# Performance work log

Measured on AMD Instinct MI355X. Metric: run time of the kernel, lower is better.

Reference implementation:

```python
import jax, jax.numpy as jnp
import numpy as np
from jax import lax

B, L, HID, H, KS, C = 2, 4096, 1024, 4, 4, 64
DH = HID // H
EPS = 1e-5


def setup_inputs():
    key = jax.random.key(0)
    ks = jax.random.split(key, 10)
    s = 0.02
    return {
        "x": jax.random.normal(ks[0], (B, L, HID), jnp.float32),
        "Wq": jax.random.normal(ks[1], (HID, HID), jnp.float32) * s,
        "Wk": jax.random.normal(ks[2], (HID, HID), jnp.float32) * s,
        "Wv": jax.random.normal(ks[3], (HID, HID), jnp.float32) * s,
        "conv_q": jax.random.normal(ks[4], (HID, 1, KS), jnp.float32) * 0.3,
        "conv_k": jax.random.normal(ks[5], (HID, 1, KS), jnp.float32) * 0.3,
        "conv_v": jax.random.normal(ks[6], (HID, 1, KS), jnp.float32) * 0.3,
        "Wbeta": jax.random.normal(ks[7], (H, HID), jnp.float32) * s,
        "rms_w": jnp.ones((HID,), jnp.float32),
        "Wo": jax.random.normal(ks[8], (HID, HID), jnp.float32) * s,
    }


def _silu(x):
    return x * jax.nn.sigmoid(x)


def _conv_act(x, w):
    # depthwise causal conv1d: torch pads both sides by KS-1 then truncates to L,
    # which equals left-pad KS-1 + valid conv. Then SiLU (as in _calculate_conv).
    y = lax.conv_general_dilated(x.transpose(0, 2, 1), w, (1,), [(KS - 1, 0)],
                                 feature_group_count=HID,
                                 dimension_numbers=('NCH', 'OIH', 'NCH'))
    return _silu(y).transpose(0, 2, 1)


def _l2norm(x):
    # matches F.normalize(p=2, dim=-1) with eps=1e-12
    return x / jnp.maximum(jnp.linalg.norm(x, axis=-1, keepdims=True), 1e-12)


def _chunk_delta_rule(Q, K, V, beta):
    b, l, h, d = Q.shape
    n = (l + C - 1) // C
    pad = n * C - l
    if pad:
        padw = ((0, 0), (0, pad), (0, 0), (0, 0))
        Q, K, V, beta = (jnp.pad(a, padw) for a in (Q, K, V, beta))
    Q, K, V = (a.reshape(b, n, C, h, d) for a in (Q, K, V))
    beta = beta.reshape(b, n, C, h, 1)
    Kb, Vb = K * beta, V * beta
    # T is SUMMED over heads in the source (single shared T per chunk).
    T = -jnp.tril(jnp.einsum('bnihd,bnjhd->bnij', Kb, K), -1) + jnp.eye(C, dtype=Q.dtype)
    # forward-substitution UT transform: T[i,:i] += T[i,:] @ T[:, :i], sequentially in i
    def body(i, T):
        row = T[:, :, i, :]                                  # (b,n,C)
        prod = jnp.einsum('bnj,bnjc->bnc', row, T)
        new = jnp.where(jnp.arange(C) < i, row + prod, row)
        return T.at[:, :, i, :].set(new)
    T = lax.fori_loop(1, C, body, T)
    W = jnp.einsum('bnij,bnjhd->bnihd', T, Kb)
    U = jnp.einsum('bnij,bnjhd->bnihd', T, Vb)

    def step(S, inp):
        q_i, k_i, w_i, u0 = inp                              # each (b,C,h,d)
        # torch.einsum('bchd,bhdd->bchd', ., S) extracts diag(S) (repeated 'd')
        dS = jnp.einsum('bhdd->bhd', S)
        u_i = u0 - w_i * dS[:, None]
        o_inter = q_i * dS[:, None]
        # source: A_i = einsum('bchd,bchd->bc', q, k).tril()  (tril over batch/chunk dims!)
        A = jnp.tril(jnp.einsum('bchd,bchd->bc', q_i, k_i))
        o_intra = jnp.einsum('bc,bchd->bchd', A, u_i)
        S = S + jnp.einsum('bchd,bche->bhde', k_i, u_i)
        return S, o_inter + o_intra

    S0 = jnp.zeros((b, h, d, d), Q.dtype)
    mv = lambda a: jnp.moveaxis(a, 1, 0)                     # chunks to scan axis
    S, O = lax.scan(step, S0, (mv(Q), mv(K), mv(W), mv(U)))
    O = jnp.moveaxis(O, 0, 1).reshape(b, n * C, h, d)[:, :l]
    return O, S


def _forward(x, Wq, Wk, Wv, conv_q, conv_k, conv_v, Wbeta, rms_w, Wo):
    q = _conv_act(x @ Wq.T, conv_q).reshape(B, L, H, DH)
    k = _conv_act(x @ Wk.T, conv_k).reshape(B, L, H, DH)
    v = _conv_act(x @ Wv.T, conv_v).reshape(B, L, H, DH)
    q, k, v = _silu(q), _silu(k), _silu(v)                   # second SiLU, as in source
    q, k = _l2norm(q), _l2norm(k)
    beta = jax.nn.sigmoid(x @ Wbeta.T)[..., None]            # (B,L,H,1)
    o, S = _chunk_delta_rule(q, k, v, beta)
    o = o.reshape(B, L, HID)
    o = o * lax.rsqrt(jnp.mean(o * o, axis=-1, keepdims=True) + EPS) * rms_w
    return o @ Wo.T, S


def reference(x, Wq, Wk, Wv, conv_q, conv_k, conv_v, Wbeta, rms_w, Wo):
    return _forward(x, Wq, Wk, Wv, conv_q, conv_k, conv_v, Wbeta, rms_w, Wo)
```

## Files before the change

### kernel.cpp

```cpp
#include <hip/hip_runtime.h>
#include <hip/hip_bf16.h>

#define L_SEQ 4096
#define HID 1024
#define NH 4
#define DH 256
#define CK 64
#define BL_TOT 8192

typedef short v8s __attribute__((ext_vector_type(8)));
typedef unsigned short v8u __attribute__((ext_vector_type(8)));
typedef unsigned short v4us __attribute__((ext_vector_type(4)));
typedef float v4f __attribute__((ext_vector_type(4)));

typedef __attribute__((address_space(1))) const void* as1cv;
typedef __attribute__((address_space(3))) void* as3v;

__device__ __forceinline__ unsigned short f2bu(float f) {
    __hip_bfloat16 h = __float2bfloat16(f);
    return *(unsigned short*)&h;
}
__device__ __forceinline__ float bu2f(unsigned short u) {
    __hip_bfloat16 h = *(__hip_bfloat16*)&u;
    return __bfloat162float(h);
}
__device__ __forceinline__ void storec(float* p, float v) { *p = v; }
__device__ __forceinline__ void storec(unsigned short* p, float v) { *p = f2bu(v); }

__global__ __launch_bounds__(256) void wcvt_kernel(const float* __restrict__ s0, const float* __restrict__ s1,
                                                   const float* __restrict__ s2, const float* __restrict__ s3,
                                                   unsigned short* __restrict__ d0, unsigned short* __restrict__ d1,
                                                   unsigned short* __restrict__ d2, unsigned short* __restrict__ d3) {
    const float* s = blockIdx.y == 0 ? s0 : blockIdx.y == 1 ? s1 : blockIdx.y == 2 ? s2 : s3;
    unsigned short* d = blockIdx.y == 0 ? d0 : blockIdx.y == 1 ? d1 : blockIdx.y == 2 ? d2 : d3;
    int i = blockIdx.x * 256 + threadIdx.x;
    int stride = gridDim.x * 256;
    for (; i < HID * HID; i += stride) d[i] = f2bu(s[i]);
}

template <typename OT>
__global__ __launch_bounds__(256) void gemm_mfma(const unsigned short* __restrict__ Ah,
                                                 const unsigned short* __restrict__ Bh,
                                                 OT* __restrict__ C, int M, int N, int K) {
    __shared__ unsigned short AsH[128 * 32];
    __shared__ unsigned short BsH[128 * 32];
    const int tid = threadIdx.x;
    const int wave = tid >> 6, lane = tid & 63;
    const int quad = lane >> 4, l16 = lane & 15;
    const int m0 = blockIdx.x * 128, n0 = blockIdx.y * 128;
    const int wm = (wave >> 1) * 64, wn = (wave & 1) * 64;

    const int srow = wave * 16 + (lane >> 2);
    const int scol = (((lane & 3) ^ ((srow >> 1) & 3)) * 8);
    const unsigned short* Ag = Ah + (size_t)(m0 + srow) * K + scol;
    const unsigned short* Bg = Bh + (size_t)(n0 + srow) * K + scol;
    char* lA = (char*)AsH;
    char* lB = (char*)BsH;
    const int lbase = wave * 1024;
    const int qsw = (quad ^ ((l16 >> 1) & 3)) * 8;

    v4f acc[4][4];
#pragma unroll
    for (int a = 0; a < 4; ++a)
#pragma unroll
        for (int b = 0; b < 4; ++b) { v4f z = {0.f, 0.f, 0.f, 0.f}; acc[a][b] = z; }

    for (int k0 = 0; k0 < K; k0 += 32) {
        __syncthreads();
        __builtin_amdgcn_global_load_lds((as1cv)(Ag + k0), (as3v)(lA + lbase), 16, 0, 0);
        __builtin_amdgcn_global_load_lds((as1cv)(Ag + (size_t)64 * K + k0), (as3v)(lA + 4096 + lbase), 16, 0, 0);
        __builtin_amdgcn_global_load_lds((as1cv)(Bg + k0), (as3v)(lB + lbase), 16, 0, 0);
        __builtin_amdgcn_global_load_lds((as1cv)(Bg + (size_t)64 * K + k0), (as3v)(lB + 4096 + lbase), 16, 0, 0);
        __syncthreads();
        v8s afh[4], bfh[4];
#pragma unroll
        for (int mt = 0; mt < 4; ++mt) afh[mt] = *(const v8s*)&AsH[(wm + mt * 16 + l16) * 32 + qsw];
#pragma unroll
        for (int nt = 0; nt < 4; ++nt) bfh[nt] = *(const v8s*)&BsH[(wn + nt * 16 + l16) * 32 + qsw];
#pragma unroll
        for (int mt = 0; mt < 4; ++mt)
#pragma unroll
            for (int nt = 0; nt < 4; ++nt)
                acc[mt][nt] = __builtin_amdgcn_mfma_f32_16x16x32_bf16(afh[mt], bfh[nt], acc[mt][nt], 0, 0, 0);
    }
#pragma unroll
    for (int mt = 0; mt < 4; ++mt)
#pragma unroll
        for (int nt = 0; nt < 4; ++nt) {
            int row = m0 + wm + mt * 16 + quad * 4;
            int col = n0 + wn + nt * 16 + l16;
#pragma unroll
            for (int r = 0; r < 4; ++r)
                storec(&C[(size_t)(row + r) * N + col], acc[mt][nt][r]);
        }
}

__global__ __launch_bounds__(256) void beta_kernel(const float* __restrict__ x,
                                                   const float* __restrict__ Wb,
                                                   float* __restrict__ betaB,
                                                   unsigned short* __restrict__ xh) {
    const int t = blockIdx.x;
    const int tid = threadIdx.x;
    const int wave = tid >> 6, lane = tid & 63;
    const float* xr = x + (size_t)t * HID;
    v4f xv = *(const v4f*)(xr + tid * 4);
    v4us xp;
#pragma unroll
    for (int i = 0; i < 4; ++i) xp[i] = f2bu(xv[i]);
    *(v4us*)&xh[(size_t)t * HID + tid * 4] = xp;
    float s[4];
#pragma unroll
    for (int h = 0; h < 4; ++h) {
        v4f wv = *(const v4f*)(Wb + (size_t)h * HID + tid * 4);
        s[h] = xv[0] * wv[0] + xv[1] * wv[1] + xv[2] * wv[2] + xv[3] * wv[3];
    }
#pragma unroll
    for (int off = 32; off; off >>= 1)
#pragma unroll
        for (int h = 0; h < 4; ++h) s[h] += __shfl_down(s[h], off);
    __shared__ float red[4][4];
    if (lane == 0)
#pragma unroll
        for (int h = 0; h < 4; ++h) red[wave][h] = s[h];
    __syncthreads();
    if (tid < 4) {
        float tot = red[0][tid] + red[1][tid] + red[2][tid] + red[3][tid];
        betaB[(size_t)t * 4 + tid] = 1.f / (1.f + expf(-tot));
    }
}

__global__ __launch_bounds__(256) void conv_kernel(const unsigned short* __restrict__ G, int gstride, int pathArg,
                                                   const float* __restrict__ wq, const float* __restrict__ wk,
                                                   const float* __restrict__ wv,
                                                   unsigned short* __restrict__ Vout,
                                                   unsigned short* __restrict__ KhiO, unsigned short* __restrict__ KloO,
                                                   unsigned short* __restrict__ Qout) {
    const int p = pathArg < 0 ? (int)blockIdx.y : pathArg;
    const int yoff = pathArg < 0 ? p * 1024 : 0;
    const float* __restrict__ w = p == 0 ? wv : p == 1 ? wk : wq;
    const int bl = blockIdx.x;
    const int l = bl & (L_SEQ - 1);
    const int tid = threadIdx.x;
    const int lane = tid & 63;
    const int c4 = (tid >> 6) * 256 + lane * 4;
    v4f wrow[4];
#pragma unroll
    for (int cc = 0; cc < 4; ++cc) wrow[cc] = *(const v4f*)&w[(c4 + cc) * 4];
    v4f acc = {0.f, 0.f, 0.f, 0.f};
#pragma unroll
    for (int j = 0; j < 4; ++j) {
        int ls = l - 3 + j;
        if (ls >= 0) {
            v4us g = *(const v4us*)&G[(size_t)(bl - 3 + j) * gstride + yoff + c4];
#pragma unroll
            for (int cc = 0; cc < 4; ++cc) acc[cc] += bu2f(g[cc]) * wrow[cc][j];
        }
    }
    float vals[4];
#pragma unroll
    for (int cc = 0; cc < 4; ++cc) {
        float a = acc[cc];
        float s1 = a / (1.f + expf(-a));
        vals[cc] = s1 / (1.f + expf(-s1));
    }
    if (p >= 1) {
        float sq = vals[0] * vals[0] + vals[1] * vals[1] + vals[2] * vals[2] + vals[3] * vals[3];
#pragma unroll
        for (int off = 32; off; off >>= 1) sq += __shfl_xor(sq, off);
        float nrm = 1.f / fmaxf(sqrtf(sq), 1e-12f);
#pragma unroll
        for (int cc = 0; cc < 4; ++cc) vals[cc] *= nrm;
    }
    const size_t ob = (size_t)bl * HID + c4;
    if (p == 1) {
        v4us hv, lv;
#pragma unroll
        for (int cc = 0; cc < 4; ++cc) {
            unsigned short h = f2bu(vals[cc]);
            hv[cc] = h;
            lv[cc] = f2bu(vals[cc] - bu2f(h));
        }
        *(v4us*)&KhiO[ob] = hv;
        *(v4us*)&KloO[ob] = lv;
    } else {
        unsigned short* O = p == 0 ? Vout : Qout;
        v4us hv;
#pragma unroll
        for (int cc = 0; cc < 4; ++cc) hv[cc] = f2bu(vals[cc]);
        *(v4us*)&O[ob] = hv;
    }
}

__global__ __launch_bounds__(256) void gram_kernel(const unsigned short* __restrict__ Khi,
                                                   const unsigned short* __restrict__ Klo,
                                                   float* __restrict__ Gg) {
    const int chunk = blockIdx.x;
    const int h = blockIdx.y;
    const int tid = threadIdx.x;
    const int wave = tid >> 6, lane = tid & 63;
    const int quad = lane >> 4, l16 = lane & 15;
    __shared__ unsigned short Hs[64 * 264];
    __shared__ unsigned short Ls[64 * 264];
    const int l0 = chunk * 64;
    const int cb = h * 256;
#pragma unroll
    for (int p = 0; p < 8; ++p) {
        int row = p * 8 + (tid >> 5);
        int col = (tid & 31) * 8;
        v8u hv = *(const v8u*)(Khi + (size_t)(l0 + row) * HID + cb + col);
        v8u lv = *(const v8u*)(Klo + (size_t)(l0 + row) * HID + cb + col);
        *(v8u*)&Hs[row * 264 + col] = hv;
        *(v8u*)&Ls[row * 264 + col] = lv;
    }
    __syncthreads();
    const int wm = wave * 16;
    v4f acc[4];
#pragma unroll
    for (int nt = 0; nt < 4; ++nt) { v4f z = {0.f, 0.f, 0.f, 0.f}; acc[nt] = z; }
#pragma unroll
    for (int ks = 0; ks < 8; ++ks) {
        v8s ah = *(const v8s*)&Hs[(wm + l16) * 264 + ks * 32 + quad * 8];
        v8s al = *(const v8s*)&Ls[(wm + l16) * 264 + ks * 32 + quad * 8];
#pragma unroll
        for (int nt = 0; nt < 4; ++nt) {
            v8s bh = *(const v8s*)&Hs[(nt * 16 + l16) * 264 + ks * 32 + quad * 8];
            v8s bl = *(const v8s*)&Ls[(nt * 16 + l16) * 264 + ks * 32 + quad * 8];
            acc[nt] = __builtin_amdgcn_mfma_f32_16x16x32_bf16(ah, bh, acc[nt], 0, 0, 0);
            acc[nt] = __builtin_amdgcn_mfma_f32_16x16x32_bf16(ah, bl, acc[nt], 0, 0, 0);
            acc[nt] = __builtin_amdgcn_mfma_f32_16x16x32_bf16(al, bh, acc[nt], 0, 0, 0);
        }
    }
    float* og = Gg + ((size_t)chunk * 4 + h) * 4096;
#pragma unroll
    for (int nt = 0; nt < 4; ++nt)
#pragma unroll
        for (int r = 0; r < 4; ++r)
            og[(wm + quad * 4 + r) * 64 + nt * 16 + l16] = acc[nt][r];
}

__global__ __launch_bounds__(256) void trec_kernel(const float* __restrict__ Gg,
                                                   const float* __restrict__ betaB,
                                                   float* __restrict__ Tg) {
    const int chunk = blockIdx.x;
    const int tid = threadIdx.x;
    const int wave = tid >> 6, lane = tid & 63;
    const int quad = lane >> 4, l16 = lane & 15;
    const int wm = wave * 16;
    __shared__ unsigned short BhR[64 * 72], BlR[64 * 72];
    __shared__ unsigned short BhT[64 * 72], BlT[64 * 72];
    __shared__ unsigned short PhR[64 * 72], PlR[64 * 72];
    __shared__ float Pf[64 * 73];
    __shared__ float betS[256];
    betS[tid] = betaB[(size_t)chunk * 256 + tid];
    __syncthreads();
    const float* gg = Gg + (size_t)chunk * 4 * 4096;
#pragma unroll
    for (int s = 0; s < 16; ++s) {
        int idx = tid + 256 * s;
        int i = idx >> 6, j = idx & 63;
        float a = 0.f;
        if (i > j) {
            a = -(betS[i * 4 + 0] * gg[idx] + betS[i * 4 + 1] * gg[4096 + idx] +
                  betS[i * 4 + 2] * gg[2 * 4096 + idx] + betS[i * 4 + 3] * gg[3 * 4096 + idx]);
        }
        unsigned short ah = f2bu(a);
        unsigned short al = f2bu(a - bu2f(ah));
        BhR[i * 72 + j] = ah;
        BlR[i * 72 + j] = al;
        BhT[j * 72 + i] = ah;
        BlT[j * 72 + i] = al;
        float p = (i == j) ? 1.f : 0.f;
        Pf[i * 73 + j] = p;
        PhR[i * 72 + j] = f2bu(p);
        PlR[i * 72 + j] = 0;
    }
    __syncthreads();

    for (int st = 0; st < 6; ++st) {
        v8s aBh[2], aBl[2], aPh[2], aPl[2];
        v8s bTh[2][4], bTl[2][4];
#pragma unroll
        for (int kk = 0; kk < 2; ++kk) {
            aBh[kk] = *(const v8s*)&BhR[(wm + l16) * 72 + kk * 32 + quad * 8];
            aBl[kk] = *(const v8s*)&BlR[(wm + l16) * 72 + kk * 32 + quad * 8];
            aPh[kk] = *(const v8s*)&PhR[(wm + l16) * 72 + kk * 32 + quad * 8];
            aPl[kk] = *(const v8s*)&PlR[(wm + l16) * 72 + kk * 32 + quad * 8];
#pragma unroll
            for (int nt = 0; nt < 4; ++nt) {
                bTh[kk][nt] = *(const v8s*)&BhT[(nt * 16 + l16) * 72 + kk * 32 + quad * 8];
                bTl[kk][nt] = *(const v8s*)&BlT[(nt * 16 + l16) * 72 + kk * 32 + quad * 8];
            }
        }
        v4f accP[4], accB[4];
#pragma unroll
        for (int nt = 0; nt < 4; ++nt) {
#pragma unroll
            for (int r = 0; r < 4; ++r)
                accP[nt][r] = Pf[(wm + quad * 4 + r) * 73 + nt * 16 + l16];
            v4f z = {0.f, 0.f, 0.f, 0.f};
            accB[nt] = z;
        }
        __syncthreads();
#pragma unroll
        for (int kk = 0; kk < 2; ++kk)
#pragma unroll
            for (int nt = 0; nt < 4; ++nt) {
                accP[nt] = __builtin_amdgcn_mfma_f32_16x16x32_bf16(aPh[kk], bTh[kk][nt], accP[nt], 0, 0, 0);
                accP[nt] = __builtin_amdgcn_mfma_f32_16x16x32_bf16(aPh[kk], bTl[kk][nt], accP[nt], 0, 0, 0);
                accP[nt] = __builtin_amdgcn_mfma_f32_16x16x32_bf16(aPl[kk], bTh[kk][nt], accP[nt], 0, 0, 0);
            }
        if (st < 5) {
#pragma unroll
            for (int kk = 0; kk < 2; ++kk)
#pragma unroll
                for (int nt = 0; nt < 4; ++nt) {
                    accB[nt] = __builtin_amdgcn_mfma_f32_16x16x32_bf16(aBh[kk], bTh[kk][nt], accB[nt], 0, 0, 0);
                    accB[nt] = __builtin_amdgcn_mfma_f32_16x16x32_bf16(aBh[kk], bTl[kk][nt], accB[nt], 0, 0, 0);
                    accB[nt] = __builtin_amdgcn_mfma_f32_16x16x32_bf16(aBl[kk], bTh[kk][nt], accB[nt], 0, 0, 0);
                }
        }
#pragma unroll
        for (int nt = 0; nt < 4; ++nt)
#pragma unroll
            for (int r = 0; r < 4; ++r) {
                int row = wm + quad * 4 + r;
                int col = nt * 16 + l16;
                float pv = accP[nt][r];
                Pf[row * 73 + col] = pv;
                unsigned short ph = f2bu(pv);
                PhR[row * 72 + col] = ph;
                PlR[row * 72 + col] = f2bu(pv - bu2f(ph));
                if (st < 5) {
                    float bv = accB[nt][r];
                    unsigned short bh2 = f2bu(bv);
                    unsigned short bl2 = f2bu(bv - bu2f(bh2));
                    BhR[row * 72 + col] = bh2;
                    BlR[row * 72 + col] = bl2;
                    BhT[col * 72 + row] = bh2;
                    BlT[col * 72 + row] = bl2;
                }
            }
        __syncthreads();
    }
#pragma unroll
    for (int s = 0; s < 16; ++s) {
        int idx = tid + 256 * s;
        int i = idx >> 6, j = idx & 63;
        float t = (i == j) ? 1.f : 3.f * Pf[i * 73 + j];
        Tg[(size_t)chunk * 4096 + idx] = t;
    }
}

__global__ __launch_bounds__(256) void wu_mfma_kernel(const float* __restrict__ Tg,
                                                      const unsigned short* __restrict__ Khi,
                                                      const unsigned short* __restrict__ Vhi,
                                                      const float* __restrict__ betaB,
                                                      unsigned short* __restrict__ Wb,
                                                      unsigned short* __restrict__ Ub,
                                                      float* __restrict__ kw, float* __restrict__ ku) {
    const int chunk = blockIdx.x;
    const int h = blockIdx.y;
    const int half = blockIdx.z;
    const int tid = threadIdx.x;
    const int wave = tid >> 6, lane = tid & 63;
    const int quad = lane >> 4, l16 = lane & 15;
    const size_t l0 = (size_t)chunk * 64;
    const int f0 = h * 256 + half * 128;
    __shared__ unsigned short Th[64 * 72], Tl[64 * 72];
    __shared__ unsigned short KT[128 * 72], VT[128 * 72];
    __shared__ float betS[64];
    if (tid < 64) betS[tid] = betaB[(l0 + tid) * 4 + h];
    __syncthreads();
#pragma unroll
    for (int s = 0; s < 16; ++s) {
        int idx = tid + 256 * s;
        int c = idx >> 6, j = idx & 63;
        float v = Tg[(size_t)chunk * 4096 + idx] * betS[j];
        unsigned short hv = f2bu(v);
        Th[c * 72 + j] = hv;
        Tl[c * 72 + j] = f2bu(v - bu2f(hv));
    }
#pragma unroll
    for (int pass = 0; pass < 4; ++pass) {
        int j = pass * 16 + (tid >> 4);
        int fc = (tid & 15) * 8;
        v8u kv = *(const v8u*)(Khi + (l0 + j) * HID + f0 + fc);
        v8u vv = *(const v8u*)(Vhi + (l0 + j) * HID + f0 + fc);
#pragma unroll
        for (int i = 0; i < 8; ++i) {
            KT[(fc + i) * 72 + j] = kv[i];
            VT[(fc + i) * 72 + j] = vv[i];
        }
    }
    __syncthreads();

    const int nf = wave * 32;
    const int bb = chunk >> 6, nn = chunk & 63;
    const size_t obase = (((size_t)bb * 4 + h) * 64 + nn) * 256 + half * 128;

#pragma unroll
    for (int phase = 0; phase < 2; ++phase) {
        const unsigned short* BT = phase ? VT : KT;
        v4f acc[4][2];
#pragma unroll
        for (int mt = 0; mt < 4; ++mt)
#pragma unroll
            for (int nt = 0; nt < 2; ++nt) { v4f z = {0.f, 0.f, 0.f, 0.f}; acc[mt][nt] = z; }
#pragma unroll
        for (int k0 = 0; k0 < 64; k0 += 32) {
            v8s ah[4], al[4], bf[2];
#pragma unroll
            for (int mt = 0; mt < 4; ++mt) {
                ah[mt] = *(const v8s*)&Th[(mt * 16 + l16) * 72 + k0 + quad * 8];
                al[mt] = *(const v8s*)&Tl[(mt * 16 + l16) * 72 + k0 + quad * 8];
            }
#pragma unroll
            for (int nt = 0; nt < 2; ++nt)
                bf[nt] = *(const v8s*)&BT[(nf + nt * 16 + l16) * 72 + k0 + quad * 8];
#pragma unroll
            for (int mt = 0; mt < 4; ++mt)
#pragma unroll
                for (int nt = 0; nt < 2; ++nt) {
                    acc[mt][nt] = __builtin_amdgcn_mfma_f32_16x16x32_bf16(ah[mt], bf[nt], acc[mt][nt], 0, 0, 0);
                    acc[mt][nt] = __builtin_amdgcn_mfma_f32_16x16x32_bf16(al[mt], bf[nt], acc[mt][nt], 0, 0, 0);
                }
        }
        unsigned short* Out = phase ? Ub : Wb;
        float* kk = phase ? ku : kw;
#pragma unroll
        for (int nt = 0; nt < 2; ++nt) {
            const int fl = nf + nt * 16 + l16;
            float dot = 0.f;
#pragma unroll
            for (int mt = 0; mt < 4; ++mt)
#pragma unroll
                for (int r = 0; r < 4; ++r) {
                    const int c = mt * 16 + quad * 4 + r;
                    float wv = acc[mt][nt][r];
                    Out[(l0 + c) * HID + f0 + fl] = f2bu(wv);
                    dot += bu2f(KT[fl * 72 + c]) * wv;
                }
            dot += __shfl_xor(dot, 16);
            dot += __shfl_xor(dot, 32);
            if (quad == 0) kk[obase + fl] = dot;
        }
    }
}

__global__ __launch_bounds__(256) void scan_kernel(const float* __restrict__ kw,
                                                   const float* __restrict__ ku,
                                                   float* __restrict__ dsA) {
    const int bh = blockIdx.x;
    const int e = threadIdx.x;
    float ds = 0.f;
    for (int n = 0; n < 64; ++n) {
        size_t idx = ((size_t)bh * 64 + n) * 256 + e;
        dsA[idx] = ds;
        ds = ds * (1.f - kw[idx]) + ku[idx];
    }
}

__device__ __forceinline__ float block_sum(float v, float* red) {
#pragma unroll
    for (int off = 32; off; off >>= 1) v += __shfl_down(v, off);
    const int wave = threadIdx.x >> 6;
    if ((threadIdx.x & 63) == 0) red[wave] = v;
    __syncthreads();
    float t = red[0] + red[1] + red[2] + red[3];
    __syncthreads();
    return t;
}

__global__ __launch_bounds__(256) void o_kernel(const unsigned short* __restrict__ Qb,
                                                const unsigned short* __restrict__ Khi,
                                                const unsigned short* __restrict__ Wb,
                                                const unsigned short* __restrict__ Ub,
                                                const float* __restrict__ dsA,
                                                const float* __restrict__ rmsw,
                                                unsigned short* __restrict__ ob,
                                                unsigned short* __restrict__ ub) {
    const int bl = blockIdx.x;
    const int b = bl >> 12, l = bl & (L_SEQ - 1);
    const int n = l >> 6, cpos = l & 63;
    const int tid = threadIdx.x;
    const int hh = tid >> 6, le = (tid & 63) * 4;
    const int c4 = hh * 256 + le;
    __shared__ float red[4];
    const size_t rowb = (size_t)bl * HID;
    v4f dsv = *(const v4f*)&dsA[(((size_t)b * 4 + hh) * 64 + n) * 256 + le];
    v4us qu = *(const v4us*)&Qb[rowb + c4];
    float qv[4];
#pragma unroll
    for (int i = 0; i < 4; ++i) qv[i] = bu2f(qu[i]);
    const bool doA = (cpos <= b);
    float Aval = 0.f;
    if (doA) {
        v4us kq = *(const v4us*)&Khi[rowb + c4];
        float s = 0.f;
#pragma unroll
        for (int i = 0; i < 4; ++i) s += qv[i] * bu2f(kq[i]);
        Aval = block_sum(s, red);
    }
    v4us uu = *(const v4us*)&Ub[rowb + c4];
    v4us wu4 = *(const v4us*)&Wb[rowb + c4];
    float ss = 0.f, ov[4];
    v4us up;
#pragma unroll
    for (int i = 0; i < 4; ++i) {
        float u = bu2f(uu[i]) - bu2f(wu4[i]) * dsv[i];
        up[i] = f2bu(u);
        float o = qv[i] * dsv[i];
        if (doA) o += Aval * u;
        ov[i] = o;
        ss += o * o;
    }
    *(v4us*)&ub[rowb + c4] = up;
    float tot = block_sum(ss, red);
    float scale = rsqrtf(tot * (1.f / 1024.f) + 1e-5f);
    v4f rw = *(const v4f*)&rmsw[c4];
    v4us op;
#pragma unroll
    for (int i = 0; i < 4; ++i) op[i] = f2bu(ov[i] * scale * rw[i]);
    *(v4us*)&ob[rowb + c4] = op;
}

#define SNS 8
__global__ __launch_bounds__(256) void s_mfma_kernel(const unsigned short* __restrict__ Khi,
                                                     const unsigned short* __restrict__ Ub,
                                                     float* __restrict__ Spart) {
    const int bh = blockIdx.x;
    const int b = bh >> 2, h = bh & 3;
    const int dt = blockIdx.y;
    const int et = blockIdx.z & 1;
    const int ns = blockIdx.z >> 1;
    const int tid = threadIdx.x;
    const int wave = tid >> 6, lane = tid & 63;
    const int quad = lane >> 4, l16 = lane & 15;
    const int wm = (wave >> 1) * 64, wn = (wave & 1) * 64;
    __shared__ unsigned short Kt[128 * 40];
    __shared__ unsigned short Ut[128 * 40];
    const int cc = tid >> 3;
    const int dcol = (tid & 7) * 16;
    const size_t rowbase = (size_t)b * 4096 + (size_t)ns * 512;
    const int ck = h * 256 + dt * 128;
    const int ce = h * 256 + et * 128;
    v4f acc[4][4];
#pragma unroll
    for (int a = 0; a < 4; ++a)
#pragma unroll
        for (int c2 = 0; c2 < 4; ++c2) { v4f z = {0.f, 0.f, 0.f, 0.f}; acc[a][c2] = z; }

    for (int kt = 0; kt < 16; ++kt) {
        size_t row = rowbase + kt * 32 + cc;
        v8u k0 = *(const v8u*)(Khi + row * HID + ck + dcol);
        v8u k1 = *(const v8u*)(Khi + row * HID + ck + dcol + 8);
        v8u u0 = *(const v8u*)(Ub + row * HID + ce + dcol);
        v8u u1 = *(const v8u*)(Ub + row * HID + ce + dcol + 8);
        __syncthreads();
#pragma unroll
        for (int j = 0; j < 8; ++j) {
            Kt[(dcol + j) * 40 + cc] = k0[j];
            Kt[(dcol + 8 + j) * 40 + cc] = k1[j];
            Ut[(dcol + j) * 40 + cc] = u0[j];
            Ut[(dcol + 8 + j) * 40 + cc] = u1[j];
        }
        __syncthreads();
        v8s af[4], bf[4];
#pragma unroll
        for (int mt = 0; mt < 4; ++mt) af[mt] = *(const v8s*)&Kt[(wm + mt * 16 + l16) * 40 + quad * 8];
#pragma unroll
        for (int nt = 0; nt < 4; ++nt) bf[nt] = *(const v8s*)&Ut[(wn + nt * 16 + l16) * 40 + quad * 8];
#pragma unroll
        for (int mt = 0; mt < 4; ++mt)
#pragma unroll
            for (int nt = 0; nt < 4; ++nt)
                acc[mt][nt] = __builtin_amdgcn_mfma_f32_16x16x32_bf16(af[mt], bf[nt], acc[mt][nt], 0, 0, 0);
    }
    float* out = Spart + (size_t)ns * (8 * 256 * 256);
#pragma unroll
    for (int mt = 0; mt < 4; ++mt)
#pragma unroll
        for (int nt = 0; nt < 4; ++nt) {
            int row = dt * 128 + wm + mt * 16 + quad * 4;
            int col = et * 128 + wn + nt * 16 + l16;
#pragma unroll
            for (int r = 0; r < 4; ++r)
                out[((size_t)bh * 256 + row + r) * 256 + col] = acc[mt][nt][r];
        }
}

__global__ __launch_bounds__(256) void sreduce_kernel(const float* __restrict__ Spart,
                                                      float* __restrict__ out) {
    int i = blockIdx.x * 256 + threadIdx.x;
    float s = 0.f;
#pragma unroll
    for (int ns = 0; ns < SNS; ++ns) s += Spart[(size_t)ns * (8 * 256 * 256) + i];
    out[i] = s;
}

extern "C" void kernel_launch(void* const* d_in, const int* in_sizes, int n_in,
                              void* d_out, int out_size, void* d_ws, size_t ws_size,
                              hipStream_t stream) {
    const float* x     = (const float*)d_in[0];
    const float* Wq    = (const float*)d_in[1];
    const float* Wk    = (const float*)d_in[2];
    const float* Wv    = (const float*)d_in[3];
    const float* convq = (const float*)d_in[4];
    const float* convk = (const float*)d_in[5];
    const float* convv = (const float*)d_in[6];
    const float* Wbeta = (const float*)d_in[7];
    const float* rmsw  = (const float*)d_in[8];
    const float* Wo    = (const float*)d_in[9];

    char* ws = (char*)d_ws;
    size_t off = 0;
    auto alloc = [&](size_t bytes) {
        char* p = ws + off;
        off += (bytes + 255) & ~(size_t)255;
        return (void*)p;
    };
    const size_t MM = (size_t)HID * HID;
    unsigned short* xhi   = (unsigned short*)alloc((size_t)BL_TOT * HID * 2);
    unsigned short* Khi   = (unsigned short*)alloc((size_t)BL_TOT * HID * 2);
    unsigned short* wbQKV = (unsigned short*)alloc(3 * MM * 2);
    unsigned short* wbO   = (unsigned short*)alloc(MM * 2);
    unsigned short* Vhi   = (unsigned short*)alloc((size_t)BL_TOT * HID * 2);
    unsigned short* Wb16  = (unsigned short*)alloc((size_t)BL_TOT * HID * 2);
    unsigned short* Ub16  = (unsigned short*)alloc((size_t)BL_TOT * HID * 2);
    float* Tg    = (float*)alloc((size_t)128 * 4096 * 4);
    float* betaB = (float*)alloc((size_t)BL_TOT * 4 * 4);
    float* kwB   = (float*)alloc((size_t)8 * 64 * 256 * 4);
    float* kuB   = (float*)alloc((size_t)8 * 64 * 256 * 4);
    float* dsA   = (float*)alloc((size_t)8 * 64 * 256 * 4);
    const size_t gt_big = (size_t)BL_TOT * 3 * HID * 2;
    const size_t gt_small = (size_t)BL_TOT * HID * 2;
    const size_t spart_bytes = (size_t)SNS * 8 * 256 * 256 * 4;
    const bool big = (off + (gt_big > spart_bytes ? gt_big : spart_bytes)) <= ws_size;
    unsigned short* Gt = (unsigned short*)alloc(big ? (gt_big > spart_bytes ? gt_big : spart_bytes)
                                                    : (gt_small > spart_bytes ? gt_small : spart_bytes));

    unsigned short* Qm = xhi;
    unsigned short* ob = Qm;
    float* Spart = (float*)Gt;

    float* out0 = (float*)d_out;
    float* out1 = out0 + (size_t)BL_TOT * HID;
    unsigned short* Klo = (unsigned short*)out0;
    unsigned short* ubf = (unsigned short*)out0 + 8388608;
    float* Gg = out0 + (size_t)4400000;

    dim3 blk(256);
    dim3 ggrid(BL_TOT / 128, HID / 128);

    wcvt_kernel<<<dim3(256, 4), blk, 0, stream>>>(Wv, Wk, Wq, Wo, wbQKV, wbQKV + MM, wbQKV + 2 * MM, wbO);
    beta_kernel<<<BL_TOT, blk, 0, stream>>>(x, Wbeta, betaB, xhi);

    if (big) {
        gemm_mfma<unsigned short><<<dim3(BL_TOT / 128, 3 * HID / 128), blk, 0, stream>>>(
            xhi, wbQKV, Gt, BL_TOT, 3 * HID, HID);
        conv_kernel<<<dim3(BL_TOT, 3), blk, 0, stream>>>(Gt, 3 * HID, -1, convq, convk, convv,
                                                         Vhi, Khi, Klo, Qm);
        gram_kernel<<<dim3(128, 4), blk, 0, stream>>>(Khi, Klo, Gg);
        trec_kernel<<<128, blk, 0, stream>>>(Gg, betaB, Tg);
    } else {
        gemm_mfma<unsigned short><<<ggrid, blk, 0, stream>>>(xhi, wbQKV, Gt, BL_TOT, HID, HID);
        conv_kernel<<<dim3(BL_TOT, 1), blk, 0, stream>>>(Gt, HID, 0, convq, convk, convv, Vhi, Khi, Klo, Qm);
        gemm_mfma<unsigned short><<<ggrid, blk, 0, stream>>>(xhi, wbQKV + MM, Gt, BL_TOT, HID, HID);
        conv_kernel<<<dim3(BL_TOT, 1), blk, 0, stream>>>(Gt, HID, 1, convq, convk, convv, Vhi, Khi, Klo, Qm);
        gram_kernel<<<dim3(128, 4), blk, 0, stream>>>(Khi, Klo, Gg);
        trec_kernel<<<128, blk, 0, stream>>>(Gg, betaB, Tg);
        gemm_mfma<unsigned short><<<ggrid, blk, 0, stream>>>(xhi, wbQKV + 2 * MM, Gt, BL_TOT, HID, HID);
        conv_kernel<<<dim3(BL_TOT, 1), blk, 0, stream>>>(Gt, HID, 2, convq, convk, convv, Vhi, Khi, Klo, Qm);
    }

    wu_mfma_kernel<<<dim3(128, 4, 2), blk, 0, stream>>>(Tg, Khi, Vhi, betaB, Wb16, Ub16, kwB, kuB);
    scan_kernel<<<8, blk, 0, stream>>>(kwB, kuB, dsA);
    o_kernel<<<BL_TOT, blk, 0, stream>>>(Qm, Khi, Wb16, Ub16, dsA, rmsw, ob, ubf);
    s_mfma_kernel<<<dim3(8, 2, 2 * SNS), blk, 0, stream>>>(Khi, ubf, Spart);
    sreduce_kernel<<<2048, blk, 0, stream>>>(Spart, out1);

    gemm_mfma<float><<<ggrid, blk, 0, stream>>>(ob, wbO, out0, BL_TOT, HID, HID);
}
```

Before: 369.9 us.

## Double GEMM K-tile to 64 and use one wave per row in beta/o kernels

The bf16 MFMA GEMM now stages 64-wide K tiles with a new 8-way XOR swizzle, halving the number of barrier pairs per K loop at the cost of twice the LDS per block. The beta and output-norm kernels are restructured so each wave handles a full row, replacing block-level shared-memory reductions and __syncthreads with wave shuffles and launching a quarter as many blocks. These changes target barrier and launch overhead in the GEMMs and the row-wise elementwise kernels, but they raise per-thread register use.

```diff
diff --git a/kernel.cpp b/kernel.cpp
--- a/kernel.cpp
+++ b/kernel.cpp
@@ -42,22 +42,21 @@
 __global__ __launch_bounds__(256) void gemm_mfma(const unsigned short* __restrict__ Ah,
                                                  const unsigned short* __restrict__ Bh,
                                                  OT* __restrict__ C, int M, int N, int K) {
-    __shared__ unsigned short AsH[128 * 32];
-    __shared__ unsigned short BsH[128 * 32];
+    __shared__ unsigned short AsH[128 * 64];
+    __shared__ unsigned short BsH[128 * 64];
     const int tid = threadIdx.x;
     const int wave = tid >> 6, lane = tid & 63;
     const int quad = lane >> 4, l16 = lane & 15;
     const int m0 = blockIdx.x * 128, n0 = blockIdx.y * 128;
     const int wm = (wave >> 1) * 64, wn = (wave & 1) * 64;
 
-    const int srow = wave * 16 + (lane >> 2);
-    const int scol = (((lane & 3) ^ ((srow >> 1) & 3)) * 8);
+    const int srow = wave * 8 + (lane >> 3);
+    const int scol = (((lane & 7) ^ (lane >> 3)) * 8);
     const unsigned short* Ag = Ah + (size_t)(m0 + srow) * K + scol;
     const unsigned short* Bg = Bh + (size_t)(n0 + srow) * K + scol;
     char* lA = (char*)AsH;
     char* lB = (char*)BsH;
     const int lbase = wave * 1024;
-    const int qsw = (quad ^ ((l16 >> 1) & 3)) * 8;
 
     v4f acc[4][4];
 #pragma unroll
@@ -65,23 +64,36 @@
 #pragma unroll
         for (int b = 0; b < 4; ++b) { v4f z = {0.f, 0.f, 0.f, 0.f}; acc[a][b] = z; }
 
-    for (int k0 = 0; k0 < K; k0 += 32) {
+    for (int k0 = 0; k0 < K; k0 += 64) {
         __syncthreads();
-        __builtin_amdgcn_global_load_lds((as1cv)(Ag + k0), (as3v)(lA + lbase), 16, 0, 0);
-        __builtin_amdgcn_global_load_lds((as1cv)(Ag + (size_t)64 * K + k0), (as3v)(lA + 4096 + lbase), 16, 0, 0);
-        __builtin_amdgcn_global_load_lds((as1cv)(Bg + k0), (as3v)(lB + lbase), 16, 0, 0);
-        __builtin_amdgcn_global_load_lds((as1cv)(Bg + (size_t)64 * K + k0), (as3v)(lB + 4096 + lbase), 16, 0, 0);
+#pragma unroll
+        for (int i = 0; i < 4; ++i)
+            __builtin_amdgcn_global_load_lds((as1cv)(Ag + (size_t)(i * 32) * K + k0),
+                                             (as3v)(lA + i * 4096 + lbase), 16, 0, 0);
+#pragma unroll
+        for (int i = 0; i < 4; ++i)
+            __builtin_amdgcn_global_load_lds((as1cv)(Bg + (size_t)(i * 32) * K + k0),
+                                             (as3v)(lB + i * 4096 + lbase), 16, 0, 0);
         __syncthreads();
-        v8s afh[4], bfh[4];
-#pragma unroll
-        for (int mt = 0; mt < 4; ++mt) afh[mt] = *(const v8s*)&AsH[(wm + mt * 16 + l16) * 32 + qsw];
-#pragma unroll
-        for (int nt = 0; nt < 4; ++nt) bfh[nt] = *(const v8s*)&BsH[(wn + nt * 16 + l16) * 32 + qsw];
-#pragma unroll
-        for (int mt = 0; mt < 4; ++mt)
-#pragma unroll
-            for (int nt = 0; nt < 4; ++nt)
-                acc[mt][nt] = __builtin_amdgcn_mfma_f32_16x16x32_bf16(afh[mt], bfh[nt], acc[mt][nt], 0, 0, 0);
+#pragma unroll
+        for (int kk = 0; kk < 2; ++kk) {
+            v8s afh[4], bfh[4];
+#pragma unroll
+            for (int mt = 0; mt < 4; ++mt) {
+                const int row = wm + mt * 16 + l16;
+                afh[mt] = *(const v8s*)&AsH[row * 64 + (((quad + 4 * kk) ^ (row & 7)) * 8)];
+            }
+#pragma unroll
+            for (int nt = 0; nt < 4; ++nt) {
+                const int row = wn + nt * 16 + l16;
+                bfh[nt] = *(const v8s*)&BsH[row * 64 + (((quad + 4 * kk) ^ (row & 7)) * 8)];
+            }
+#pragma unroll
+            for (int mt = 0; mt < 4; ++mt)
+#pragma unroll
+                for (int nt = 0; nt < 4; ++nt)
+                    acc[mt][nt] = __builtin_amdgcn_mfma_f32_16x16x32_bf16(afh[mt], bfh[nt], acc[mt][nt], 0, 0, 0);
+        }
     }
 #pragma unroll
     for (int mt = 0; mt < 4; ++mt)
@@ -99,34 +111,32 @@
                                                    const float* __restrict__ Wb,
                                                    float* __restrict__ betaB,
                                                    unsigned short* __restrict__ xh) {
-    const int t = blockIdx.x;
-    const int tid = threadIdx.x;
-    const int wave = tid >> 6, lane = tid & 63;
+    const int t = blockIdx.x * 4 + (threadIdx.x >> 6);
+    const int lane = threadIdx.x & 63;
     const float* xr = x + (size_t)t * HID;
-    v4f xv = *(const v4f*)(xr + tid * 4);
-    v4us xp;
-#pragma unroll
-    for (int i = 0; i < 4; ++i) xp[i] = f2bu(xv[i]);
-    *(v4us*)&xh[(size_t)t * HID + tid * 4] = xp;
-    float s[4];
-#pragma unroll
-    for (int h = 0; h < 4; ++h) {
-        v4f wv = *(const v4f*)(Wb + (size_t)h * HID + tid * 4);
-        s[h] = xv[0] * wv[0] + xv[1] * wv[1] + xv[2] * wv[2] + xv[3] * wv[3];
-    }
+    float s[4] = {0.f, 0.f, 0.f, 0.f};
+    v4f xv[4];
+#pragma unroll
+    for (int c = 0; c < 4; ++c) {
+        const int i4 = c * 256 + lane * 4;
+        xv[c] = *(const v4f*)(xr + i4);
+        v4us xp;
+#pragma unroll
+        for (int i = 0; i < 4; ++i) xp[i] = f2bu(xv[c][i]);
+        *(v4us*)&xh[(size_t)t * HID + i4] = xp;
+    }
+#pragma unroll
+    for (int h = 0; h < 4; ++h)
+#pragma unroll
+        for (int c = 0; c < 4; ++c) {
+            v4f wv = *(const v4f*)(Wb + (size_t)h * HID + c * 256 + lane * 4);
+            s[h] += xv[c][0] * wv[0] + xv[c][1] * wv[1] + xv[c][2] * wv[2] + xv[c][3] * wv[3];
+        }
 #pragma unroll
     for (int off = 32; off; off >>= 1)
 #pragma unroll
-        for (int h = 0; h < 4; ++h) s[h] += __shfl_down(s[h], off);
-    __shared__ float red[4][4];
-    if (lane == 0)
-#pragma unroll
-        for (int h = 0; h < 4; ++h) red[wave][h] = s[h];
-    __syncthreads();
-    if (tid < 4) {
-        float tot = red[0][tid] + red[1][tid] + red[2][tid] + red[3][tid];
-        betaB[(size_t)t * 4 + tid] = 1.f / (1.f + expf(-tot));
-    }
+        for (int h = 0; h < 4; ++h) s[h] += __shfl_xor(s[h], off);
+    if (lane < 4) betaB[(size_t)t * 4 + lane] = 1.f / (1.f + expf(-s[lane]));
 }
 
 __global__ __launch_bounds__(256) void conv_kernel(const unsigned short* __restrict__ G, int gstride, int pathArg,
@@ -460,17 +470,6 @@
     }
 }
 
-__device__ __forceinline__ float block_sum(float v, float* red) {
-#pragma unroll
-    for (int off = 32; off; off >>= 1) v += __shfl_down(v, off);
-    const int wave = threadIdx.x >> 6;
-    if ((threadIdx.x & 63) == 0) red[wave] = v;
-    __syncthreads();
-    float t = red[0] + red[1] + red[2] + red[3];
-    __syncthreads();
-    return t;
-}
-
 __global__ __launch_bounds__(256) void o_kernel(const unsigned short* __restrict__ Qb,
                                                 const unsigned short* __restrict__ Khi,
                                                 const unsigned short* __restrict__ Wb,
@@ -479,49 +478,65 @@
                                                 const float* __restrict__ rmsw,
                                                 unsigned short* __restrict__ ob,
                                                 unsigned short* __restrict__ ub) {
-    const int bl = blockIdx.x;
-    const int b = bl >> 12, l = bl & (L_SEQ - 1);
+    const int r = blockIdx.x * 4 + (threadIdx.x >> 6);
+    const int lane = threadIdx.x & 63;
+    const int b = r >> 12, l = r & (L_SEQ - 1);
     const int n = l >> 6, cpos = l & 63;
-    const int tid = threadIdx.x;
-    const int hh = tid >> 6, le = (tid & 63) * 4;
-    const int c4 = hh * 256 + le;
-    __shared__ float red[4];
-    const size_t rowb = (size_t)bl * HID;
-    v4f dsv = *(const v4f*)&dsA[(((size_t)b * 4 + hh) * 64 + n) * 256 + le];
-    v4us qu = *(const v4us*)&Qb[rowb + c4];
-    float qv[4];
-#pragma unroll
-    for (int i = 0; i < 4; ++i) qv[i] = bu2f(qu[i]);
+    const size_t rowb = (size_t)r * HID;
     const bool doA = (cpos <= b);
+    float qv[4][4];
+    v4f dsv[4];
+    float As = 0.f;
+#pragma unroll
+    for (int hh = 0; hh < 4; ++hh) {
+        const int c4 = hh * 256 + lane * 4;
+        dsv[hh] = *(const v4f*)&dsA[(((size_t)b * 4 + hh) * 64 + n) * 256 + lane * 4];
+        v4us qu = *(const v4us*)&Qb[rowb + c4];
+#pragma unroll
+        for (int i = 0; i < 4; ++i) qv[hh][i] = bu2f(qu[i]);
+        if (doA) {
+            v4us kq = *(const v4us*)&Khi[rowb + c4];
+#pragma unroll
+            for (int i = 0; i < 4; ++i) As += qv[hh][i] * bu2f(kq[i]);
+        }
+    }
     float Aval = 0.f;
     if (doA) {
-        v4us kq = *(const v4us*)&Khi[rowb + c4];
-        float s = 0.f;
-#pragma unroll
-        for (int i = 0; i < 4; ++i) s += qv[i] * bu2f(kq[i]);
-        Aval = block_sum(s, red);
-    }
-    v4us uu = *(const v4us*)&Ub[rowb + c4];
-    v4us wu4 = *(const v4us*)&Wb[rowb + c4];
-    float ss = 0.f, ov[4];
-    v4us up;
-#pragma unroll
-    for (int i = 0; i < 4; ++i) {
-        float u = bu2f(uu[i]) - bu2f(wu4[i]) * dsv[i];
-        up[i] = f2bu(u);
-        float o = qv[i] * dsv[i];
-        if (doA) o += Aval * u;
-        ov[i] = o;
-        ss += o * o;
-    }
-    *(v4us*)&ub[rowb + c4] = up;
-    float tot = block_sum(ss, red);
-    float scale = rsqrtf(tot * (1.f / 1024.f) + 1e-5f);
-    v4f rw = *(const v4f*)&rmsw[c4];
-    v4us op;
-#pragma unroll
-    for (int i = 0; i < 4; ++i) op[i] = f2bu(ov[i] * scale * rw[i]);
-    *(v4us*)&ob[rowb + c4] = op;
+#pragma unroll
+        for (int off = 32; off; off >>= 1) As += __shfl_xor(As, off);
+        Aval = As;
+    }
+    float ss = 0.f;
+    float ov[4][4];
+#pragma unroll
+    for (int hh = 0; hh < 4; ++hh) {
+        const int c4 = hh * 256 + lane * 4;
+        v4us uu = *(const v4us*)&Ub[rowb + c4];
+        v4us wu4 = *(const v4us*)&Wb[rowb + c4];
+        v4us up;
+#pragma unroll
+        for (int i = 0; i < 4; ++i) {
+            float u = bu2f(uu[i]) - bu2f(wu4[i]) * dsv[hh][i];
+            up[i] = f2bu(u);
+            float o = qv[hh][i] * dsv[hh][i];
+            if (doA) o += Aval * u;
+            ov[hh][i] = o;
+            ss += o * o;
+        }
+        *(v4us*)&ub[rowb + c4] = up;
+    }
+#pragma unroll
+    for (int off = 32; off; off >>= 1) ss += __shfl_xor(ss, off);
+    float scale = rsqrtf(ss * (1.f / 1024.f) + 1e-5f);
+#pragma unroll
+    for (int hh = 0; hh < 4; ++hh) {
+        const int c4 = hh * 256 + lane * 4;
+        v4f rw = *(const v4f*)&rmsw[c4];
+        v4us op;
+#pragma unroll
+        for (int i = 0; i < 4; ++i) op[i] = f2bu(ov[hh][i] * scale * rw[i]);
+        *(v4us*)&ob[rowb + c4] = op;
+    }
 }
 
 #define SNS 8
@@ -653,7 +668,7 @@
     dim3 ggrid(BL_TOT / 128, HID / 128);
 
     wcvt_kernel<<<dim3(256, 4), blk, 0, stream>>>(Wv, Wk, Wq, Wo, wbQKV, wbQKV + MM, wbQKV + 2 * MM, wbO);
-    beta_kernel<<<BL_TOT, blk, 0, stream>>>(x, Wbeta, betaB, xhi);
+    beta_kernel<<<BL_TOT / 4, blk, 0, stream>>>(x, Wbeta, betaB, xhi);
 
     if (big) {
         gemm_mfma<unsigned short><<<dim3(BL_TOT / 128, 3 * HID / 128), blk, 0, stream>>>(
@@ -675,7 +690,7 @@
 
     wu_mfma_kernel<<<dim3(128, 4, 2), blk, 0, stream>>>(Tg, Khi, Vhi, betaB, Wb16, Ub16, kwB, kuB);
     scan_kernel<<<8, blk, 0, stream>>>(kwB, kuB, dsA);
-    o_kernel<<<BL_TOT, blk, 0, stream>>>(Qm, Khi, Wb16, Ub16, dsA, rmsw, ob, ubf);
+    o_kernel<<<BL_TOT / 4, blk, 0, stream>>>(Qm, Khi, Wb16, Ub16, dsA, rmsw, ob, ubf);
     s_mfma_kernel<<<dim3(8, 2, 2 * SNS), blk, 0, stream>>>(Khi, ubf, Spart);
     sreduce_kernel<<<2048, blk, 0, stream>>>(Spart, out1);
 
```

New measurement: 366.4 us. About the same (-0.9%).
